# Performance work log

Hardware: AMD Instinct MI355X
Metric: run time of the kernel (lower is better)

The kernel has to match this reference:

```python
import jax, jax.numpy as jnp
import numpy as np

NUM_NODES = 100000
NUM_EDGES = 3_200_000
WALKS_PER_NODE = 4
WALK_LENGTH = 8
SKIP_FIRST = True


def setup_inputs() -> dict:
    key = jax.random.key(0)
    k1, k2, k3 = jax.random.split(key, 3)
    edge_index = jax.random.randint(k1, (2, NUM_EDGES), 0, NUM_NODES, dtype=jnp.int32)
    edge_weight = jax.random.uniform(k2, (NUM_EDGES,), dtype=jnp.float32)
    # one uniform per walker per step; S = NUM_NODES * WALKS_PER_NODE
    rand_unif = jax.random.uniform(k3, (NUM_NODES * WALKS_PER_NODE, WALK_LENGTH), dtype=jnp.float32)
    return {"edge_index": edge_index, "edge_weight": edge_weight, "rand_unif": rand_unif}


def _random_walk_edges(edge_index, rand_unif):
    """Returns added [2, S*L] edges (root -> walked node), int dtype."""
    row, col = edge_index[0], edge_index[1]
    # is_sorted=False path: sort edges by source to build CSR
    order = jnp.argsort(row)
    row_s = row[order]
    col_s = col[order]
    deg = jax.ops.segment_sum(jnp.ones_like(row_s), row_s, num_segments=NUM_NODES)  # [N]
    rowptr = jnp.concatenate([jnp.zeros((1,), deg.dtype), jnp.cumsum(deg)])  # [N+1]
    # start = all nodes, repeated walks_per_node times
    start = jnp.tile(jnp.arange(NUM_NODES, dtype=row.dtype), WALKS_PER_NODE)  # [S]

    def step(cur, u):
        d = deg[cur]  # [S]
        off = jnp.minimum((u * d.astype(u.dtype)).astype(cur.dtype), jnp.maximum(d - 1, 0))
        nxt = jnp.where(d > 0, col_s[rowptr[cur] + off], cur)  # stay if isolated
        return nxt, nxt

    _, walks = jax.lax.scan(step, start, rand_unif.T)  # [L_total, S]
    walks = walks.T  # [S, WALK_LENGTH] == n_id[:, 1:]
    k = 1 if SKIP_FIRST else 0  # skip_first drops the first-hop node (n_id[:, 2:])
    targets = walks[:, k:]  # [S, L]
    L = targets.shape[1]
    roots = jnp.broadcast_to(start[:, None], (start.shape[0], L))
    return jnp.stack([roots.reshape(-1), targets.reshape(-1)])  # [2, S*L]


def reference(edge_index, edge_weight, rand_unif):
    added = _random_walk_edges(edge_index, rand_unif)
    out_edge_index = jnp.concatenate([edge_index, added], axis=1)
    added_w = jnp.ones((added.shape[1],), edge_weight.dtype)
    out_edge_weight = jnp.concatenate([edge_weight, added_w])
    return out_edge_index, out_edge_weight
```

## Files before the change

### kernel.cpp

```cpp
#include <hip/hip_runtime.h>

#define ARW_N_NODES   100000
#define ARW_N_EDGES   3200000
#define ARW_N_WALKERS 400000
#define ARW_WLEN      8
#define ARW_LOUT      7
#define ARW_ROW_LEN   6000000
#define ARW_OUT_ELEMS 18000000

#define ARW_NB    256
#define ARW_RPB   392
#define ARW_NT    3125
#define ARW_TP    3136
#define ARW_TILE  1024
#define ARW_TPB   5
#define ARW_PMAX  14336

#define ARW_HT    0
#define ARW_BT    900000
#define ARW_TOT   1750000
#define ARW_CB    1760000
#define ARW_PD    1800000
#define ARW_P     6000000
#define ARW_COLS  12000000

__global__ void AddRandomWalkEdge_16896401342869_kernel() {}

__global__ __launch_bounds__(1024) void arw16896_thist(const int* __restrict__ row,
                                                       int* __restrict__ s) {
    __shared__ int h[ARW_TPB * 256];
    int tid = threadIdx.x;
    for (int x = tid; x < ARW_TPB * 256; x += 1024) h[x] = 0;
    __syncthreads();
    int base_e = blockIdx.x * (ARW_TPB * ARW_TILE) + tid;
    #pragma unroll
    for (int j = 0; j < ARW_TPB; j++)
        atomicAdd(&h[j * 256 + (row[base_e + j * 1024] / ARW_RPB)], 1);
    __syncthreads();
    for (int x = tid; x < ARW_TPB * ARW_NB; x += 1024) {
        int b = x / ARW_TPB, j = x % ARW_TPB;
        s[ARW_HT + b * ARW_TP + blockIdx.x * ARW_TPB + j] = h[j * 256 + b];
    }
}

__global__ __launch_bounds__(1024) void arw16896_bscan2(int* __restrict__ s) {
    __shared__ int wsum[16];
    int b = blockIdx.x, tid = threadIdx.x, lane = tid & 63, wid = tid >> 6;
    int carry = 0;
    for (int c0 = 0; c0 < ARW_NT; c0 += 1024) {
        int t = c0 + tid;
        int v = (t < ARW_NT) ? s[ARW_HT + b * ARW_TP + t] : 0;
        int sv = v;
        #pragma unroll
        for (int off = 1; off < 64; off <<= 1) {
            int x = __shfl_up(sv, off, 64);
            if (lane >= off) sv += x;
        }
        if (lane == 63) wsum[wid] = sv;
        __syncthreads();
        int pre = 0, tot = 0;
        #pragma unroll
        for (int w = 0; w < 16; w++) {
            int x = wsum[w];
            if (w < wid) pre += x;
            tot += x;
        }
        if (t < ARW_NT) s[ARW_BT + b * ARW_TP + t] = carry + pre + sv - v;
        carry += tot;
        __syncthreads();
    }
    if (tid == 0) s[ARW_TOT + b] = carry;
}

__global__ __launch_bounds__(256) void arw16896_bbase(int* __restrict__ s) {
    __shared__ int sm[256];
    int tid = threadIdx.x;
    int v = s[ARW_TOT + tid];
    sm[tid] = v;
    __syncthreads();
    for (int off = 1; off < 256; off <<= 1) {
        int x = 0;
        if (tid >= off) x = sm[tid - off];
        __syncthreads();
        sm[tid] += x;
        __syncthreads();
    }
    s[ARW_CB + tid] = sm[tid] - v;
}

__global__ __launch_bounds__(1024) void arw16896_part(const int* __restrict__ row,
                                                      const int* __restrict__ col,
                                                      int* __restrict__ s) {
    __shared__ unsigned W[16 * 256];
    int tid  = threadIdx.x;
    int wave = tid >> 6, lane = tid & 63;
    int e = blockIdx.x * ARW_TILE + tid;
    int r = row[e], cv = col[e];
    int b = r / ARW_RPB;
    int lr = r - b * ARW_RPB;
    W[tid] = 0; W[tid + 1024] = 0; W[tid + 2048] = 0; W[tid + 3072] = 0;
    __syncthreads();
    unsigned long long mask = ~0ULL;
    #pragma unroll
    for (int bit = 0; bit < 8; bit++) {
        unsigned long long bal = __ballot((b >> bit) & 1);
        mask &= ((b >> bit) & 1) ? bal : ~bal;
    }
    int rankw = __popcll(mask & ((1ULL << lane) - 1ULL));
    W[wave * 256 + b] = (unsigned)__popcll(mask);
    __syncthreads();
    int cross = 0;
    for (int w2 = 0; w2 < 16; w2++) {
        if (w2 >= wave) break;
        cross += (int)W[w2 * 256 + b];
    }
    int base = s[ARW_CB + b] + s[ARW_BT + b * ARW_TP + blockIdx.x];
    s[ARW_P + base + cross + rankw] = (lr << 17) | cv;
}

__global__ __launch_bounds__(1024) void arw16896_pass2(int* __restrict__ s) {
    __shared__ int PL[ARW_PMAX];
    __shared__ unsigned short W[16 * 512];
    __shared__ int hist[512], pref[512], runc[512];
    int tid = threadIdx.x, lane = tid & 63, wave = tid >> 6;
    int b = blockIdx.x;
    int start = s[ARW_CB + b];
    int end   = (b == ARW_NB - 1) ? ARW_N_EDGES : s[ARW_CB + b + 1];
    int cnt = end - start;
    int staged = cnt < ARW_PMAX ? cnt : ARW_PMAX;
    int rows0 = b * ARW_RPB;
    int nrows = ARW_N_NODES - rows0; if (nrows > ARW_RPB) nrows = ARW_RPB;

    for (int k = tid; k < staged; k += 1024) PL[k] = s[ARW_P + start + k];
    if (tid < 512) hist[tid] = 0;
    __syncthreads();

    for (int k = tid; k < cnt; k += 1024) {
        unsigned p = (unsigned)(k < staged ? PL[k] : s[ARW_P + start + k]);
        atomicAdd(&hist[p >> 17], 1);
    }
    __syncthreads();
    if (tid < 512) pref[tid] = hist[tid];
    __syncthreads();
    for (int off = 1; off < 512; off <<= 1) {
        int x = 0;
        if (tid < 512 && tid >= off) x = pref[tid - off];
        __syncthreads();
        if (tid < 512) pref[tid] += x;
        __syncthreads();
    }
    if (tid < 512) runc[tid] = 0;
    if (tid < nrows) {
        unsigned deg = (unsigned)hist[tid];
        unsigned rp  = (unsigned)(start + pref[tid] - hist[tid]);
        s[ARW_PD + rows0 + tid] = (int)((rp << 10) | deg);
    }
    __syncthreads();

    for (int c0 = 0; c0 < cnt; c0 += 1024) {
        int k = c0 + tid;
        int valid = (k < cnt) ? 1 : 0;
        unsigned p = 0u;
        if (valid) p = (unsigned)(k < staged ? PL[k] : s[ARW_P + start + k]);
        unsigned lr = p >> 17;
        #pragma unroll
        for (int j = 0; j < 8; j++) W[tid + j * 1024] = 0;
        __syncthreads();
        unsigned long long mask = ~0ULL;
        #pragma unroll
        for (int bit = 0; bit < 9; bit++) {
            unsigned long long bal = __ballot((lr >> bit) & 1u);
            mask &= ((lr >> bit) & 1u) ? bal : ~bal;
        }
        mask &= __ballot(valid);
        int rankw = __popcll(mask & ((1ULL << lane) - 1ULL));
        if (valid) W[wave * 512 + lr] = (unsigned short)__popcll(mask);
        __syncthreads();
        if (valid) {
            int cross = 0;
            for (int w2 = 0; w2 < 16; w2++) {
                if (w2 >= wave) break;
                cross += (int)W[w2 * 512 + lr];
            }
            int pos = start + (pref[lr] - hist[lr]) + runc[lr] + cross + rankw;
            s[ARW_COLS + pos] = (int)(p & 0x1FFFFu);
        }
        __syncthreads();
        if (tid < 512) {
            int a = 0;
            #pragma unroll
            for (int w = 0; w < 16; w++) a += (int)W[w * 512 + tid];
            runc[tid] += a;
        }
        __syncthreads();
    }
}

__global__ __launch_bounds__(256) void arw16896_walk(const float* __restrict__ ru,
                                                     const int* __restrict__ ei,
                                                     const int* __restrict__ s,
                                                     float* __restrict__ o) {
    __shared__ float tg[4 * 256 * ARW_LOUT];
    int tid = threadIdx.x;
    int v = blockIdx.x * 256 + tid;
    if (v < ARW_N_NODES) {
        float uu[4][8];
        int cur[4];
        #pragma unroll
        for (int k = 0; k < 4; k++) {
            const float4* rp4 = (const float4*)(ru + (size_t)(v + k * ARW_N_NODES) * 8);
            float4 ra = rp4[0], rb = rp4[1];
            uu[k][0] = ra.x; uu[k][1] = ra.y; uu[k][2] = ra.z; uu[k][3] = ra.w;
            uu[k][4] = rb.x; uu[k][5] = rb.y; uu[k][6] = rb.z; uu[k][7] = rb.w;
        }
        unsigned pd0 = (unsigned)s[ARW_PD + v];
        int d0  = (int)(pd0 & 1023u);
        int rp0 = (int)(pd0 >> 10);
        #pragma unroll
        for (int k = 0; k < 4; k++) {
            int off = (int)(uu[k][0] * (float)d0);
            if (off > d0 - 1) off = d0 - 1;
            int nxt = s[ARW_COLS + rp0 + off];
            cur[k] = (d0 > 0) ? nxt : v;
        }
        #pragma unroll
        for (int t = 1; t < ARW_WLEN; t++) {
            unsigned pdk[4];
            #pragma unroll
            for (int k = 0; k < 4; k++) pdk[k] = (unsigned)s[ARW_PD + cur[k]];
            #pragma unroll
            for (int k = 0; k < 4; k++) {
                int d = (int)(pdk[k] & 1023u);
                int off = (int)(uu[k][t] * (float)d);
                if (off > d - 1) off = d - 1;
                int nxt = s[ARW_COLS + (int)(pdk[k] >> 10) + off];
                cur[k] = (d > 0) ? nxt : cur[k];
                tg[k * (256 * ARW_LOUT) + tid * ARW_LOUT + (t - 1)] = (float)cur[k];
            }
        }
    }
    __syncthreads();
    int blkN = ARW_N_NODES - blockIdx.x * 256;
    if (blkN > 256) blkN = 256;
    int valid = blkN * ARW_LOUT;
    #pragma unroll
    for (int k = 0; k < 4; k++) {
        int base = ARW_ROW_LEN + ARW_N_EDGES +
                   (k * ARW_N_NODES + blockIdx.x * 256) * ARW_LOUT;
        for (int j = tid; j < valid; j += 256)
            o[base + j] = tg[k * (256 * ARW_LOUT) + j];
    }
    int gid = blockIdx.x * 256 + tid;
    int stride = gridDim.x * 256;
    for (int i4 = gid; i4 < ARW_N_EDGES / 4; i4 += stride) {
        int4 r1 = ((const int4*)(ei + ARW_N_EDGES))[i4];
        ((float4*)(o + ARW_ROW_LEN))[i4] =
            make_float4((float)r1.x, (float)r1.y, (float)r1.z, (float)r1.w);
    }
    for (int i4 = gid; i4 < (ARW_N_WALKERS * ARW_LOUT) / 4; i4 += stride) {
        int i = i4 * 4;
        float4 r;
        r.x = (float)(((i    ) / ARW_LOUT) % ARW_N_NODES);
        r.y = (float)(((i + 1) / ARW_LOUT) % ARW_N_NODES);
        r.z = (float)(((i + 2) / ARW_LOUT) % ARW_N_NODES);
        r.w = (float)(((i + 3) / ARW_LOUT) % ARW_N_NODES);
        ((float4*)(o + ARW_N_EDGES))[i4] = r;
    }
}

__global__ __launch_bounds__(256) void arw16896_asm(const int* __restrict__ ei,
                                                    const float* __restrict__ wgt,
                                                    float* __restrict__ o) {
    int i4 = blockIdx.x * blockDim.x + threadIdx.x;
    if (i4 < ARW_N_EDGES / 4) {
        int4 r0 = ((const int4*)ei)[i4];
        float4 wv = ((const float4*)wgt)[i4];
        ((float4*)o)[i4] = make_float4((float)r0.x, (float)r0.y, (float)r0.z, (float)r0.w);
        ((float4*)(o + 2 * ARW_ROW_LEN))[i4] = wv;
    }
    if (i4 < (ARW_N_WALKERS * ARW_LOUT) / 4) {
        ((float4*)(o + 2 * ARW_ROW_LEN + ARW_N_EDGES))[i4] = make_float4(1.f, 1.f, 1.f, 1.f);
    }
}

extern "C" void kernel_launch(void* const* d_in, const int* in_sizes, int n_in,
                              void* d_out, int out_size, void* d_ws, size_t ws_size,
                              hipStream_t stream) {
    const int*   ei  = (const int*)d_in[0];
    const float* wgt = (const float*)d_in[1];
    const float* ru  = (const float*)d_in[2];
    int*   s = (int*)d_out;
    float* o = (float*)d_out;
    const int* row = ei;
    const int* col = ei + ARW_N_EDGES;

    arw16896_thist <<<ARW_NT / ARW_TPB, 1024, 0, stream>>>(row, s);
    arw16896_bscan2<<<ARW_NB, 1024, 0, stream>>>(s);
    arw16896_bbase <<<1, 256, 0, stream>>>(s);
    arw16896_part  <<<ARW_NT, 1024, 0, stream>>>(row, col, s);
    arw16896_pass2 <<<ARW_NB, 1024, 0, stream>>>(s);
    arw16896_walk  <<<(ARW_N_NODES + 255) / 256, 256, 0, stream>>>(ru, ei, s, o);
    arw16896_asm   <<<(ARW_N_EDGES / 4 + 255) / 256, 256, 0, stream>>>(ei, wgt, o);
}
```

Baseline: 234.8 us.

## Partition pass2 bucket scatter into per-wave contiguous chunks with per-wave row offsets

The CSR bucket pass now gives each wavefront a contiguous slice of the bucket's packed edges. It first counts per-row, per-wave occurrences with ballot-based leader updates, then prefix-scans them into per-wave row bases. The scatter then runs entirely within each wave, using a leader read-and-increment plus a shuffle. This removes the per-1024-chunk block-wide barriers and shared W-table resets, and it keeps the stable ordering. In exchange it drops the LDS staging of the input, so each edge is read from global memory twice. It also relies on a 16-bit count per row per wave.

```diff
diff --git a/kernel.cpp b/kernel.cpp
--- a/kernel.cpp
+++ b/kernel.cpp
@@ -14,7 +14,6 @@
 #define ARW_TP    3136
 #define ARW_TILE  1024
 #define ARW_TPB   5
-#define ARW_PMAX  14336
 
 #define ARW_HT    0
 #define ARW_BT    900000
@@ -119,25 +118,44 @@
 }
 
 __global__ __launch_bounds__(1024) void arw16896_pass2(int* __restrict__ s) {
-    __shared__ int PL[ARW_PMAX];
-    __shared__ unsigned short W[16 * 512];
-    __shared__ int hist[512], pref[512], runc[512];
+    __shared__ unsigned short C[ARW_RPB * 16];
+    __shared__ int B[ARW_RPB * 16];
+    __shared__ int hist[512], pref[512];
     int tid = threadIdx.x, lane = tid & 63, wave = tid >> 6;
     int b = blockIdx.x;
     int start = s[ARW_CB + b];
     int end   = (b == ARW_NB - 1) ? ARW_N_EDGES : s[ARW_CB + b + 1];
     int cnt = end - start;
-    int staged = cnt < ARW_PMAX ? cnt : ARW_PMAX;
     int rows0 = b * ARW_RPB;
     int nrows = ARW_N_NODES - rows0; if (nrows > ARW_RPB) nrows = ARW_RPB;
-
-    for (int k = tid; k < staged; k += 1024) PL[k] = s[ARW_P + start + k];
+    int per  = (cnt + 15) >> 4;
+    int wbeg = wave * per; if (wbeg > cnt) wbeg = cnt;
+    int wend = wbeg + per; if (wend > cnt) wend = cnt;
+
+    for (int x = tid; x < ARW_RPB * 16; x += 1024) C[x] = 0;
     if (tid < 512) hist[tid] = 0;
     __syncthreads();
 
-    for (int k = tid; k < cnt; k += 1024) {
-        unsigned p = (unsigned)(k < staged ? PL[k] : s[ARW_P + start + k]);
-        atomicAdd(&hist[p >> 17], 1);
+    for (int k = wbeg + lane; k < wend; k += 64) {
+        unsigned lr = (unsigned)s[ARW_P + start + k] >> 17;
+        unsigned long long mask = ~0ULL;
+        #pragma unroll
+        for (int bit = 0; bit < 9; bit++) {
+            unsigned long long bal = __ballot((lr >> bit) & 1u);
+            mask &= ((lr >> bit) & 1u) ? bal : ~bal;
+        }
+        mask &= __ballot(1);
+        int leader = __ffsll(mask) - 1;
+        if (lane == leader)
+            C[lr * 16 + wave] = (unsigned short)(C[lr * 16 + wave] + __popcll(mask));
+    }
+    __syncthreads();
+
+    if (tid < nrows) {
+        int a = 0;
+        #pragma unroll
+        for (int w = 0; w < 16; w++) a += (int)C[tid * 16 + w];
+        hist[tid] = a;
     }
     __syncthreads();
     if (tid < 512) pref[tid] = hist[tid];
@@ -149,50 +167,34 @@
         if (tid < 512) pref[tid] += x;
         __syncthreads();
     }
-    if (tid < 512) runc[tid] = 0;
     if (tid < nrows) {
-        unsigned deg = (unsigned)hist[tid];
-        unsigned rp  = (unsigned)(start + pref[tid] - hist[tid]);
-        s[ARW_PD + rows0 + tid] = (int)((rp << 10) | deg);
-    }
-    __syncthreads();
-
-    for (int c0 = 0; c0 < cnt; c0 += 1024) {
-        int k = c0 + tid;
-        int valid = (k < cnt) ? 1 : 0;
-        unsigned p = 0u;
-        if (valid) p = (unsigned)(k < staged ? PL[k] : s[ARW_P + start + k]);
+        int rowbase = start + pref[tid] - hist[tid];
+        s[ARW_PD + rows0 + tid] = (int)(((unsigned)rowbase << 10) | (unsigned)hist[tid]);
+        int acc = rowbase;
+        #pragma unroll
+        for (int w = 0; w < 16; w++) { B[tid * 16 + w] = acc; acc += (int)C[tid * 16 + w]; }
+    }
+    __syncthreads();
+
+    for (int k = wbeg + lane; k < wend; k += 64) {
+        unsigned p = (unsigned)s[ARW_P + start + k];
         unsigned lr = p >> 17;
-        #pragma unroll
-        for (int j = 0; j < 8; j++) W[tid + j * 1024] = 0;
-        __syncthreads();
         unsigned long long mask = ~0ULL;
         #pragma unroll
         for (int bit = 0; bit < 9; bit++) {
             unsigned long long bal = __ballot((lr >> bit) & 1u);
             mask &= ((lr >> bit) & 1u) ? bal : ~bal;
         }
-        mask &= __ballot(valid);
+        mask &= __ballot(1);
+        int leader = __ffsll(mask) - 1;
         int rankw = __popcll(mask & ((1ULL << lane) - 1ULL));
-        if (valid) W[wave * 512 + lr] = (unsigned short)__popcll(mask);
-        __syncthreads();
-        if (valid) {
-            int cross = 0;
-            for (int w2 = 0; w2 < 16; w2++) {
-                if (w2 >= wave) break;
-                cross += (int)W[w2 * 512 + lr];
-            }
-            int pos = start + (pref[lr] - hist[lr]) + runc[lr] + cross + rankw;
-            s[ARW_COLS + pos] = (int)(p & 0x1FFFFu);
-        }
-        __syncthreads();
-        if (tid < 512) {
-            int a = 0;
-            #pragma unroll
-            for (int w = 0; w < 16; w++) a += (int)W[w * 512 + tid];
-            runc[tid] += a;
-        }
-        __syncthreads();
+        int base = 0;
+        if (lane == leader) {
+            base = B[lr * 16 + wave];
+            B[lr * 16 + wave] = base + __popcll(mask);
+        }
+        base = __shfl(base, leader, 64);
+        s[ARW_COLS + base + rankw] = (int)(p & 0x1FFFFu);
     }
 }
 
```

Result: no change. 238.1 us (+1.4%).

## Enlarge partition tiles to 4096 edges and simplify the bucket scan to one pass

Applied to the files above, without the earlier changes.

Each partition tile now covers 4096 edges, processed in four rounds of 1024 with per-bucket running counters held in shared memory, so there are 782 tiles instead of 3125. The histogram is stored tile-major, and the per-bucket scan fits in a single 1024-thread pass with no carry loop. This cuts the histogram and scan traffic and the number of blocks. In exchange the part kernel gains extra barriers per round, and scatter locality may change.

```diff
diff --git a/kernel.cpp b/kernel.cpp
--- a/kernel.cpp
+++ b/kernel.cpp
@@ -10,10 +10,9 @@
 
 #define ARW_NB    256
 #define ARW_RPB   392
-#define ARW_NT    3125
-#define ARW_TP    3136
-#define ARW_TILE  1024
-#define ARW_TPB   5
+#define ARW_NT    782
+#define ARW_TP    784
+#define ARW_TILE  4096
 #define ARW_PMAX  14336
 
 #define ARW_HT    0
@@ -28,48 +27,40 @@
 
 __global__ __launch_bounds__(1024) void arw16896_thist(const int* __restrict__ row,
                                                        int* __restrict__ s) {
-    __shared__ int h[ARW_TPB * 256];
-    int tid = threadIdx.x;
-    for (int x = tid; x < ARW_TPB * 256; x += 1024) h[x] = 0;
-    __syncthreads();
-    int base_e = blockIdx.x * (ARW_TPB * ARW_TILE) + tid;
-    #pragma unroll
-    for (int j = 0; j < ARW_TPB; j++)
-        atomicAdd(&h[j * 256 + (row[base_e + j * 1024] / ARW_RPB)], 1);
-    __syncthreads();
-    for (int x = tid; x < ARW_TPB * ARW_NB; x += 1024) {
-        int b = x / ARW_TPB, j = x % ARW_TPB;
-        s[ARW_HT + b * ARW_TP + blockIdx.x * ARW_TPB + j] = h[j * 256 + b];
-    }
+    __shared__ int h[256];
+    int tid = threadIdx.x, t = blockIdx.x;
+    if (tid < 256) h[tid] = 0;
+    __syncthreads();
+    #pragma unroll
+    for (int rnd = 0; rnd < 4; rnd++) {
+        int e = t * ARW_TILE + rnd * 1024 + tid;
+        if (e < ARW_N_EDGES) atomicAdd(&h[row[e] / ARW_RPB], 1);
+    }
+    __syncthreads();
+    if (tid < 256) s[ARW_HT + t * 256 + tid] = h[tid];
 }
 
 __global__ __launch_bounds__(1024) void arw16896_bscan2(int* __restrict__ s) {
     __shared__ int wsum[16];
     int b = blockIdx.x, tid = threadIdx.x, lane = tid & 63, wid = tid >> 6;
-    int carry = 0;
-    for (int c0 = 0; c0 < ARW_NT; c0 += 1024) {
-        int t = c0 + tid;
-        int v = (t < ARW_NT) ? s[ARW_HT + b * ARW_TP + t] : 0;
-        int sv = v;
-        #pragma unroll
-        for (int off = 1; off < 64; off <<= 1) {
-            int x = __shfl_up(sv, off, 64);
-            if (lane >= off) sv += x;
-        }
-        if (lane == 63) wsum[wid] = sv;
-        __syncthreads();
-        int pre = 0, tot = 0;
-        #pragma unroll
-        for (int w = 0; w < 16; w++) {
-            int x = wsum[w];
-            if (w < wid) pre += x;
-            tot += x;
-        }
-        if (t < ARW_NT) s[ARW_BT + b * ARW_TP + t] = carry + pre + sv - v;
-        carry += tot;
-        __syncthreads();
-    }
-    if (tid == 0) s[ARW_TOT + b] = carry;
+    int v = (tid < ARW_NT) ? s[ARW_HT + tid * 256 + b] : 0;
+    int sv = v;
+    #pragma unroll
+    for (int off = 1; off < 64; off <<= 1) {
+        int x = __shfl_up(sv, off, 64);
+        if (lane >= off) sv += x;
+    }
+    if (lane == 63) wsum[wid] = sv;
+    __syncthreads();
+    int pre = 0, tot = 0;
+    #pragma unroll
+    for (int w = 0; w < 16; w++) {
+        int x = wsum[w];
+        if (w < wid) pre += x;
+        tot += x;
+    }
+    if (tid < ARW_NT) s[ARW_BT + b * ARW_TP + tid] = pre + sv - v;
+    if (tid == 0) s[ARW_TOT + b] = tot;
 }
 
 __global__ __launch_bounds__(256) void arw16896_bbase(int* __restrict__ s) {
@@ -91,31 +82,54 @@
 __global__ __launch_bounds__(1024) void arw16896_part(const int* __restrict__ row,
                                                       const int* __restrict__ col,
                                                       int* __restrict__ s) {
-    __shared__ unsigned W[16 * 256];
+    __shared__ unsigned short W[16 * 256];
+    __shared__ int runc[256], lbase[256];
     int tid  = threadIdx.x;
     int wave = tid >> 6, lane = tid & 63;
-    int e = blockIdx.x * ARW_TILE + tid;
-    int r = row[e], cv = col[e];
-    int b = r / ARW_RPB;
-    int lr = r - b * ARW_RPB;
-    W[tid] = 0; W[tid + 1024] = 0; W[tid + 2048] = 0; W[tid + 3072] = 0;
-    __syncthreads();
-    unsigned long long mask = ~0ULL;
-    #pragma unroll
-    for (int bit = 0; bit < 8; bit++) {
-        unsigned long long bal = __ballot((b >> bit) & 1);
-        mask &= ((b >> bit) & 1) ? bal : ~bal;
-    }
-    int rankw = __popcll(mask & ((1ULL << lane) - 1ULL));
-    W[wave * 256 + b] = (unsigned)__popcll(mask);
-    __syncthreads();
-    int cross = 0;
-    for (int w2 = 0; w2 < 16; w2++) {
-        if (w2 >= wave) break;
-        cross += (int)W[w2 * 256 + b];
-    }
-    int base = s[ARW_CB + b] + s[ARW_BT + b * ARW_TP + blockIdx.x];
-    s[ARW_P + base + cross + rankw] = (lr << 17) | cv;
+    int t = blockIdx.x;
+    if (tid < 256) {
+        runc[tid]  = 0;
+        lbase[tid] = s[ARW_CB + tid] + s[ARW_BT + tid * ARW_TP + t];
+    }
+    __syncthreads();
+    #pragma unroll
+    for (int rnd = 0; rnd < 4; rnd++) {
+        int e = t * ARW_TILE + rnd * 1024 + tid;
+        int valid = (e < ARW_N_EDGES) ? 1 : 0;
+        int r = valid ? row[e] : 0;
+        int cv = valid ? col[e] : 0;
+        int b = r / ARW_RPB;
+        int lr = r - b * ARW_RPB;
+        #pragma unroll
+        for (int j = 0; j < 4; j++) W[tid + j * 1024] = 0;
+        __syncthreads();
+        unsigned long long mask = ~0ULL;
+        #pragma unroll
+        for (int bit = 0; bit < 8; bit++) {
+            unsigned long long bal = __ballot((b >> bit) & 1);
+            mask &= ((b >> bit) & 1) ? bal : ~bal;
+        }
+        mask &= __ballot(valid);
+        int rankw = __popcll(mask & ((1ULL << lane) - 1ULL));
+        if (valid) W[wave * 256 + b] = (unsigned short)__popcll(mask);
+        __syncthreads();
+        if (valid) {
+            int cross = 0;
+            for (int w2 = 0; w2 < 16; w2++) {
+                if (w2 >= wave) break;
+                cross += (int)W[w2 * 256 + b];
+            }
+            s[ARW_P + lbase[b] + runc[b] + cross + rankw] = (lr << 17) | cv;
+        }
+        __syncthreads();
+        if (tid < 256) {
+            int a = 0;
+            #pragma unroll
+            for (int w = 0; w < 16; w++) a += (int)W[w * 256 + tid];
+            runc[tid] += a;
+        }
+        __syncthreads();
+    }
 }
 
 __global__ __launch_bounds__(1024) void arw16896_pass2(int* __restrict__ s) {
@@ -294,7 +308,7 @@
     const int* row = ei;
     const int* col = ei + ARW_N_EDGES;
 
-    arw16896_thist <<<ARW_NT / ARW_TPB, 1024, 0, stream>>>(row, s);
+    arw16896_thist <<<ARW_NT, 1024, 0, stream>>>(row, s);
     arw16896_bscan2<<<ARW_NB, 1024, 0, stream>>>(s);
     arw16896_bbase <<<1, 256, 0, stream>>>(s);
     arw16896_part  <<<ARW_NT, 1024, 0, stream>>>(row, col, s);
```

Measured after the change: 228.4 us. 1.03x faster.
